# Performance work log

Measured on AMD Instinct MI355X. Metric: run time of the kernel, lower is better.

The kernel has to match this reference:

```python
import jax, jax.numpy as jnp
import numpy as np


def setup_inputs() -> dict:
    key = jax.random.key(0)
    k1, k2 = jax.random.split(key)
    mutation_dist = jax.random.uniform(k1, (8192, 96), dtype=jnp.float32)
    train_data = jax.random.uniform(k2, (65536, 96), dtype=jnp.float32)
    return {"mutation_dist": mutation_dist, "train_data": train_data}


def reference(mutation_dist, train_data):
    # torch.cdist with default p=2: pairwise Euclidean distances [N, M]
    # default compute_mode for large inputs)
    x2 = jnp.sum(mutation_dist * mutation_dist, axis=-1, keepdims=True)   # [N,1]
    y2 = jnp.sum(train_data * train_data, axis=-1)[None, :]               # [1,M]
    xy = mutation_dist @ train_data.T                                     # [N,M]
    sq = jnp.maximum(x2 + y2 - 2.0 * xy, 0.0)
    distances = jnp.sqrt(sq)
    min_dist = jnp.min(distances, axis=1) * 10.0
    return min_dist
```

## Files before the change

### kernel.cpp

```cpp
#include <hip/hip_runtime.h>
#include <hip/hip_bf16.h>


typedef __attribute__((ext_vector_type(8))) short bf16x8;
typedef __attribute__((ext_vector_type(4))) float f32x4;
typedef __attribute__((ext_vector_type(4))) int i32x4;
typedef __attribute__((ext_vector_type(16))) int i32x16;

#define NQ 8192
#define NT 65536
#define KD 96
#define QB 512
#define TSPLIT 64
#define TCHUNK (NT / TSPLIT)
#define TTILE 64
#define TILES (TCHUNK / TTILE)

#define GLOAD_LDS16(gp, lp)                                                  \
  __builtin_amdgcn_global_load_lds(                                          \
      (const __attribute__((address_space(1))) unsigned int*)(gp),           \
      (__attribute__((address_space(3))) unsigned int*)(lp), 16, 0, 0)
#define GLOAD_LDS4(gp, lp)                                                   \
  __builtin_amdgcn_global_load_lds(                                          \
      (const __attribute__((address_space(1))) unsigned int*)(gp),           \
      (__attribute__((address_space(3))) unsigned int*)(lp), 4, 0, 0)

static __device__ __forceinline__ ushort f2bf(float f) {
  unsigned u = __float_as_uint(f);
  return (ushort)((u + 0x7fffu + ((u >> 16) & 1u)) >> 16);
}
static __device__ __forceinline__ unsigned pk2(float a, float b) {
  return (unsigned)f2bf(a) | ((unsigned)f2bf(b) << 16);
}
static __device__ __forceinline__ int imin(int a, int b) { return a < b ? a : b; }

__global__ __launch_bounds__(256) void prep_kernel(
    const float* __restrict__ qf, const float* __restrict__ tf,
    char* __restrict__ qi8, char* __restrict__ ti8,
    int* __restrict__ x2i, int* __restrict__ y2h,
    float* __restrict__ outp)
{
  const int tid = threadIdx.x;
  const int b = blockIdx.x;
  const bool isq = b < (NQ / 64);
  const int rb = isq ? b : b - (NQ / 64);
  const float4* src = (const float4*)((isq ? qf : tf) + (size_t)rb * 64 * KD);
  char* drow = (isq ? qi8 : ti8) + (size_t)rb * 64 * KD;
  const int rloc = tid >> 2;
  const int t = tid & 3;

  unsigned pk[6];
  int sn = 0;
  #pragma unroll
  for (int i = 0; i < 6; ++i) {
    float4 v = src[tid * 6 + i];
    int q0 = (int)rintf(v.x * 254.0f) - 127;
    int q1 = (int)rintf(v.y * 254.0f) - 127;
    int q2 = (int)rintf(v.z * 254.0f) - 127;
    int q3 = (int)rintf(v.w * 254.0f) - 127;
    sn += q0 * q0 + q1 * q1 + q2 * q2 + q3 * q3;
    int w0 = isq ? q0 : -q0, w1 = isq ? q1 : -q1;
    int w2 = isq ? q2 : -q2, w3 = isq ? q3 : -q3;
    pk[i] = (unsigned)(w0 & 255) | ((unsigned)(w1 & 255) << 8) |
            ((unsigned)(w2 & 255) << 16) | ((unsigned)(w3 & 255) << 24);
  }
  uint2* op = (uint2*)(drow + (size_t)rloc * KD + t * 24);
  op[0] = make_uint2(pk[0], pk[1]);
  op[1] = make_uint2(pk[2], pk[3]);
  op[2] = make_uint2(pk[4], pk[5]);

  sn += __shfl_xor(sn, 1, 64);
  sn += __shfl_xor(sn, 2, 64);
  if (t == 0) {
    int row = rb * 64 + rloc;
    if (isq) { x2i[row] = sn; outp[row] = __uint_as_float(0x7f800000u); }
    else     { y2h[row] = (sn + 1) >> 1; }
  }
}

__global__ __launch_bounds__(512) void min_dist_kernel(
    const char* __restrict__ qi8, const char* __restrict__ ti8,
    const int* __restrict__ x2i, const int* __restrict__ y2h,
    float* __restrict__ outp)
{
  __shared__ __align__(16) char ldsA[2][TTILE * KD];
  __shared__ __align__(16) int ldsY[2][TTILE];

  const int tid  = threadIdx.x;
  const int w    = tid >> 6;
  const int lane = tid & 63;
  const int col  = lane & 31;
  const int hi   = lane >> 5;
  const int tsplit = blockIdx.x & (TSPLIT - 1);
  const int qblock = blockIdx.x / TSPLIT;
  const int qbase  = qblock * QB + w * 64;

  i32x4 bq[2][3];
  #pragma unroll
  for (int ct = 0; ct < 2; ++ct) {
    const char* qp = qi8 + (size_t)(qbase + ct * 32 + col) * KD + hi * 16;
    #pragma unroll
    for (int kb = 0; kb < 3; ++kb)
      bq[ct][kb] = *(const volatile i32x4*)(qp + kb * 32);
  }

  int goff, loff;
  {
    int f = tid >> 6, l = tid & 63;
    int tt = f / 3, kb = f - tt * 3;
    goff = (tt * 32 + (l & 31)) * KD + kb * 32 + (l >> 5) * 16;
    loff = tid * 16;
  }

  int m0 = 0x7fffffff, m1 = 0x7fffffff;

  const int trow0 = tsplit * TCHUNK;

  {
    const char* g0 = ti8 + (size_t)trow0 * KD;
    if (tid < 384)
      GLOAD_LDS16(g0 + goff, &ldsA[0][loff]);
    if (w == 0)
      GLOAD_LDS4(y2h + trow0 + lane, &ldsY[0][lane]);
  }
  __syncthreads();

  int cur = 0;
  #pragma unroll 1
  for (int tile = 0; tile < TILES; ++tile) {
    if (tile + 1 < TILES) {
      const int tb2 = trow0 + (tile + 1) * TTILE;
      const char* g2 = ti8 + (size_t)tb2 * KD;
      if (tid < 384)
        GLOAD_LDS16(g2 + goff, &ldsA[cur ^ 1][loff]);
      if (w == 0)
        GLOAD_LDS4(y2h + tb2 + lane, &ldsY[cur ^ 1][lane]);
    }

    #pragma unroll
    for (int tt = 0; tt < 2; ++tt) {
      const char* ap = &ldsA[cur][tt * 3 * 1024 + lane * 16];
      i32x4 a0 = *(const i32x4*)(ap);
      i32x4 a1 = *(const i32x4*)(ap + 1024);
      i32x4 a2 = *(const i32x4*)(ap + 2048);

      i32x4 y0 = *(const i32x4*)&ldsY[cur][tt * 32 + hi * 4];
      i32x4 y1 = *(const i32x4*)&ldsY[cur][tt * 32 + hi * 4 + 8];
      i32x4 yq2 = *(const i32x4*)&ldsY[cur][tt * 32 + hi * 4 + 16];
      i32x4 yq3 = *(const i32x4*)&ldsY[cur][tt * 32 + hi * 4 + 24];
      i32x16 c;
      c[0] = y0[0];  c[1] = y0[1];  c[2] = y0[2];  c[3] = y0[3];
      c[4] = y1[0];  c[5] = y1[1];  c[6] = y1[2];  c[7] = y1[3];
      c[8] = yq2[0]; c[9] = yq2[1]; c[10] = yq2[2]; c[11] = yq2[3];
      c[12] = yq3[0]; c[13] = yq3[1]; c[14] = yq3[2]; c[15] = yq3[3];

      i32x16 acc0 = __builtin_amdgcn_mfma_i32_32x32x32_i8(a0, bq[0][0], c, 0, 0, 0);
      i32x16 acc1 = __builtin_amdgcn_mfma_i32_32x32x32_i8(a0, bq[1][0], c, 0, 0, 0);
      acc0 = __builtin_amdgcn_mfma_i32_32x32x32_i8(a1, bq[0][1], acc0, 0, 0, 0);
      acc1 = __builtin_amdgcn_mfma_i32_32x32x32_i8(a1, bq[1][1], acc1, 0, 0, 0);
      acc0 = __builtin_amdgcn_mfma_i32_32x32x32_i8(a2, bq[0][2], acc0, 0, 0, 0);
      acc1 = __builtin_amdgcn_mfma_i32_32x32x32_i8(a2, bq[1][2], acc1, 0, 0, 0);

      {
        int t0 = imin(imin(acc0[0], acc0[1]), imin(acc0[2], acc0[3]));
        int t1 = imin(imin(acc0[4], acc0[5]), imin(acc0[6], acc0[7]));
        int t2 = imin(imin(acc0[8], acc0[9]), imin(acc0[10], acc0[11]));
        int t3 = imin(imin(acc0[12], acc0[13]), imin(acc0[14], acc0[15]));
        m0 = imin(m0, imin(imin(t0, t1), imin(t2, t3)));
      }
      {
        int t0 = imin(imin(acc1[0], acc1[1]), imin(acc1[2], acc1[3]));
        int t1 = imin(imin(acc1[4], acc1[5]), imin(acc1[6], acc1[7]));
        int t2 = imin(imin(acc1[8], acc1[9]), imin(acc1[10], acc1[11]));
        int t3 = imin(imin(acc1[12], acc1[13]), imin(acc1[14], acc1[15]));
        m1 = imin(m1, imin(imin(t0, t1), imin(t2, t3)));
      }
    }

    __syncthreads();
    cur ^= 1;
  }

  m0 = imin(m0, __shfl_xor(m0, 32, 64));
  m1 = imin(m1, __shfl_xor(m1, 32, 64));
  if (hi == 0) {
    int q0 = qbase + col;
    int sq0 = x2i[q0] + (m0 << 1);
    if (sq0 < 0) sq0 = 0;
    atomicMin((unsigned int*)&outp[q0],
              __float_as_uint(sqrtf((float)sq0) * (10.0f / 254.0f)));
    int q1 = qbase + 32 + col;
    int sq1 = x2i[q1] + (m1 << 1);
    if (sq1 < 0) sq1 = 0;
    atomicMin((unsigned int*)&outp[q1],
              __float_as_uint(sqrtf((float)sq1) * (10.0f / 254.0f)));
  }
}

extern "C" void kernel_launch(void* const* d_in, const int* in_sizes, int n_in,
                              void* d_out, int out_size, void* d_ws, size_t ws_size,
                              hipStream_t stream) {
  const float* qf = (const float*)d_in[0];
  const float* tf = (const float*)d_in[1];
  float* outp = (float*)d_out;

  char* qi8 = (char*)d_ws;
  char* ti8 = qi8 + (size_t)NQ * KD;
  int* x2i = (int*)(ti8 + (size_t)NT * KD);
  int* y2h = x2i + NQ;

  prep_kernel<<<(NQ + NT) / 64, 256, 0, stream>>>(qf, tf, qi8, ti8, x2i, y2h, outp);
  min_dist_kernel<<<(NQ / QB) * TSPLIT, 512, 0, stream>>>(qi8, ti8, x2i, y2h, outp);
}
```

Measured before the change: 119.3 us.

## Fuse prep and min-distance into one cooperative kernel with grid sync

Merges the quantization prep kernel and the int8 MFMA min-distance kernel into one cooperative launch separated by a grid-wide barrier, which removes the second kernel launch and its gap. The T split is halved to 32 so the grid of 512 blocks can be co-resident, with a 4-blocks-per-CU launch bound. Each block now does twice as many tiles and there is less parallelism over T. Grid sync adds its own overhead, and a two-kernel fallback runs if the cooperative launch fails.

New measurement: 200.3 us. 67.9% more time.

```diff
diff --git a/kernel.cpp b/kernel.cpp
--- a/kernel.cpp
+++ b/kernel.cpp
@@ -1,5 +1,8 @@
 #include <hip/hip_runtime.h>
 #include <hip/hip_bf16.h>
+#include <hip/hip_cooperative_groups.h>
+
+namespace cg = cooperative_groups;
 
 
 typedef __attribute__((ext_vector_type(8))) short bf16x8;
@@ -11,10 +14,13 @@
 #define NT 65536
 #define KD 96
 #define QB 512
-#define TSPLIT 64
+#define TSPLIT 32
 #define TCHUNK (NT / TSPLIT)
 #define TTILE 64
 #define TILES (TCHUNK / TTILE)
+#define GRID ((NQ / QB) * TSPLIT)
+#define PREP_ROWS ((NQ + NT) / GRID)
+#define PREP_UNITS (PREP_ROWS * 4)
 
 #define GLOAD_LDS16(gp, lp)                                                  \
   __builtin_amdgcn_global_load_lds(                                          \
@@ -34,65 +40,65 @@
 }
 static __device__ __forceinline__ int imin(int a, int b) { return a < b ? a : b; }
 
-__global__ __launch_bounds__(256) void prep_kernel(
+static __device__ __forceinline__ void phase1_prep(
+    int b, int tid,
     const float* __restrict__ qf, const float* __restrict__ tf,
     char* __restrict__ qi8, char* __restrict__ ti8,
     int* __restrict__ x2i, int* __restrict__ y2h,
     float* __restrict__ outp)
 {
-  const int tid = threadIdx.x;
-  const int b = blockIdx.x;
-  const bool isq = b < (NQ / 64);
-  const int rb = isq ? b : b - (NQ / 64);
-  const float4* src = (const float4*)((isq ? qf : tf) + (size_t)rb * 64 * KD);
-  char* drow = (isq ? qi8 : ti8) + (size_t)rb * 64 * KD;
-  const int rloc = tid >> 2;
-  const int t = tid & 3;
-
-  unsigned pk[6];
-  int sn = 0;
-  #pragma unroll
-  for (int i = 0; i < 6; ++i) {
-    float4 v = src[tid * 6 + i];
-    int q0 = (int)rintf(v.x * 254.0f) - 127;
-    int q1 = (int)rintf(v.y * 254.0f) - 127;
-    int q2 = (int)rintf(v.z * 254.0f) - 127;
-    int q3 = (int)rintf(v.w * 254.0f) - 127;
-    sn += q0 * q0 + q1 * q1 + q2 * q2 + q3 * q3;
-    int w0 = isq ? q0 : -q0, w1 = isq ? q1 : -q1;
-    int w2 = isq ? q2 : -q2, w3 = isq ? q3 : -q3;
-    pk[i] = (unsigned)(w0 & 255) | ((unsigned)(w1 & 255) << 8) |
-            ((unsigned)(w2 & 255) << 16) | ((unsigned)(w3 & 255) << 24);
-  }
-  uint2* op = (uint2*)(drow + (size_t)rloc * KD + t * 24);
-  op[0] = make_uint2(pk[0], pk[1]);
-  op[1] = make_uint2(pk[2], pk[3]);
-  op[2] = make_uint2(pk[4], pk[5]);
-
-  sn += __shfl_xor(sn, 1, 64);
-  sn += __shfl_xor(sn, 2, 64);
-  if (t == 0) {
-    int row = rb * 64 + rloc;
-    if (isq) { x2i[row] = sn; outp[row] = __uint_as_float(0x7f800000u); }
-    else     { y2h[row] = (sn + 1) >> 1; }
-  }
-}
-
-__global__ __launch_bounds__(512) void min_dist_kernel(
+  #pragma unroll 2
+  for (int u = tid; u < PREP_UNITS; u += 512) {
+    const int rl = u >> 2;
+    const int t  = u & 3;
+    const int gr = b * PREP_ROWS + rl;
+    const bool isq = gr < NQ;
+    const int r = isq ? gr : gr - NQ;
+    const float4* src = (const float4*)((isq ? qf : tf) + (size_t)r * KD);
+    char* drow = (isq ? qi8 : ti8) + (size_t)r * KD;
+
+    unsigned pk[6];
+    int sn = 0;
+    #pragma unroll
+    for (int i = 0; i < 6; ++i) {
+      float4 v = src[t * 6 + i];
+      int q0 = (int)rintf(v.x * 254.0f) - 127;
+      int q1 = (int)rintf(v.y * 254.0f) - 127;
+      int q2 = (int)rintf(v.z * 254.0f) - 127;
+      int q3 = (int)rintf(v.w * 254.0f) - 127;
+      sn += q0 * q0 + q1 * q1 + q2 * q2 + q3 * q3;
+      int w0 = isq ? q0 : -q0, w1 = isq ? q1 : -q1;
+      int w2 = isq ? q2 : -q2, w3 = isq ? q3 : -q3;
+      pk[i] = (unsigned)(w0 & 255) | ((unsigned)(w1 & 255) << 8) |
+              ((unsigned)(w2 & 255) << 16) | ((unsigned)(w3 & 255) << 24);
+    }
+    uint2* op = (uint2*)(drow + t * 24);
+    op[0] = make_uint2(pk[0], pk[1]);
+    op[1] = make_uint2(pk[2], pk[3]);
+    op[2] = make_uint2(pk[4], pk[5]);
+
+    sn += __shfl_xor(sn, 1, 64);
+    sn += __shfl_xor(sn, 2, 64);
+    if (t == 0) {
+      if (isq) { x2i[r] = sn; outp[r] = __uint_as_float(0x7f800000u); }
+      else     { y2h[r] = (sn + 1) >> 1; }
+    }
+  }
+}
+
+static __device__ __forceinline__ void phase2_mindist(
+    int b, int tid,
+    char (*ldsA)[TTILE * KD], int (*ldsY)[TTILE],
     const char* __restrict__ qi8, const char* __restrict__ ti8,
     const int* __restrict__ x2i, const int* __restrict__ y2h,
     float* __restrict__ outp)
 {
-  __shared__ __align__(16) char ldsA[2][TTILE * KD];
-  __shared__ __align__(16) int ldsY[2][TTILE];
-
-  const int tid  = threadIdx.x;
   const int w    = tid >> 6;
   const int lane = tid & 63;
   const int col  = lane & 31;
   const int hi   = lane >> 5;
-  const int tsplit = blockIdx.x & (TSPLIT - 1);
-  const int qblock = blockIdx.x / TSPLIT;
+  const int tsplit = b & (TSPLIT - 1);
+  const int qblock = b / TSPLIT;
   const int qbase  = qblock * QB + w * 64;
 
   i32x4 bq[2][3];
@@ -197,6 +203,37 @@
   }
 }
 
+__global__ __launch_bounds__(512, 4) void fused_kernel(
+    const float* __restrict__ qf, const float* __restrict__ tf,
+    char* __restrict__ qi8, char* __restrict__ ti8,
+    int* __restrict__ x2i, int* __restrict__ y2h,
+    float* __restrict__ outp)
+{
+  __shared__ __align__(16) char ldsA[2][TTILE * KD];
+  __shared__ __align__(16) int ldsY[2][TTILE];
+  phase1_prep(blockIdx.x, threadIdx.x, qf, tf, qi8, ti8, x2i, y2h, outp);
+  cg::this_grid().sync();
+  phase2_mindist(blockIdx.x, threadIdx.x, ldsA, ldsY, qi8, ti8, x2i, y2h, outp);
+}
+
+__global__ __launch_bounds__(512, 4) void prep_split(
+    const float* __restrict__ qf, const float* __restrict__ tf,
+    char* __restrict__ qi8, char* __restrict__ ti8,
+    int* __restrict__ x2i, int* __restrict__ y2h,
+    float* __restrict__ outp)
+{
+  phase1_prep(blockIdx.x, threadIdx.x, qf, tf, qi8, ti8, x2i, y2h, outp);
+}
+__global__ __launch_bounds__(512, 4) void mind_split(
+    const char* __restrict__ qi8, const char* __restrict__ ti8,
+    const int* __restrict__ x2i, const int* __restrict__ y2h,
+    float* __restrict__ outp)
+{
+  __shared__ __align__(16) char ldsA[2][TTILE * KD];
+  __shared__ __align__(16) int ldsY[2][TTILE];
+  phase2_mindist(blockIdx.x, threadIdx.x, ldsA, ldsY, qi8, ti8, x2i, y2h, outp);
+}
+
 extern "C" void kernel_launch(void* const* d_in, const int* in_sizes, int n_in,
                               void* d_out, int out_size, void* d_ws, size_t ws_size,
                               hipStream_t stream) {
@@ -209,6 +246,14 @@
   int* x2i = (int*)(ti8 + (size_t)NT * KD);
   int* y2h = x2i + NQ;
 
-  prep_kernel<<<(NQ + NT) / 64, 256, 0, stream>>>(qf, tf, qi8, ti8, x2i, y2h, outp);
-  min_dist_kernel<<<(NQ / QB) * TSPLIT, 512, 0, stream>>>(qi8, ti8, x2i, y2h, outp);
-}
+  void* args[] = {(void*)&qf, (void*)&tf, (void*)&qi8, (void*)&ti8,
+                  (void*)&x2i, (void*)&y2h, (void*)&outp};
+  hipError_t err = hipLaunchCooperativeKernel((const void*)fused_kernel,
+                                              dim3(GRID), dim3(512),
+                                              args, 0, stream);
+  if (err != hipSuccess) {
+    (void)hipGetLastError();
+    prep_split<<<GRID, 512, 0, stream>>>(qf, tf, qi8, ti8, x2i, y2h, outp);
+    mind_split<<<GRID, 512, 0, stream>>>(qi8, ti8, x2i, y2h, outp);
+  }
+}
```

## Prefetch two tiles ahead with vmcnt-based waits and split loader waves

Applied to the files above, without the earlier changes.

Changes the double-buffered tile loop so two tiles are already in flight before the loop. Each iteration waits with s_waitcnt vmcnt(1) and a raw barrier instead of a full __syncthreads, and issues the load for tile+2 after the compute barrier. The y2h load moves from wave 0 to wave 6, so no wave issues both kinds of async LDS load, and the vmcnt count stays simple. It also adds an explicit wait for the query register loads. This gives the global loads more time to complete behind compute. In exchange it depends on hand-written waitcnt correctness and issues wraparound (wasted) loads on the last two iterations.

Result: no change. 119.8 us (+0.4%).

```diff
diff --git a/kernel.cpp b/kernel.cpp
--- a/kernel.cpp
+++ b/kernel.cpp
@@ -103,12 +103,12 @@
     for (int kb = 0; kb < 3; ++kb)
       bq[ct][kb] = *(const volatile i32x4*)(qp + kb * 32);
   }
-
-  int goff, loff;
-  {
-    int f = tid >> 6, l = tid & 63;
-    int tt = f / 3, kb = f - tt * 3;
-    goff = (tt * 32 + (l & 31)) * KD + kb * 32 + (l >> 5) * 16;
+  asm volatile("s_waitcnt vmcnt(0)" ::: "memory");
+
+  int goff = 0, loff = 0;
+  if (w < 6) {
+    int tt = w / 3, kb = w - tt * 3;
+    goff = (tt * 32 + col) * KD + kb * 32 + hi * 16;
     loff = tid * 16;
   }
 
@@ -116,26 +116,20 @@
 
   const int trow0 = tsplit * TCHUNK;
 
-  {
-    const char* g0 = ti8 + (size_t)trow0 * KD;
-    if (tid < 384)
-      GLOAD_LDS16(g0 + goff, &ldsA[0][loff]);
-    if (w == 0)
-      GLOAD_LDS4(y2h + trow0 + lane, &ldsY[0][lane]);
-  }
-  __syncthreads();
+  #pragma unroll
+  for (int p = 0; p < 2; ++p) {
+    const int tb = trow0 + p * TTILE;
+    if (w < 6)      GLOAD_LDS16(ti8 + (size_t)tb * KD + goff, &ldsA[p][loff]);
+    else if (w == 6) GLOAD_LDS4(y2h + tb + lane, &ldsY[p][lane]);
+  }
 
   int cur = 0;
   #pragma unroll 1
   for (int tile = 0; tile < TILES; ++tile) {
-    if (tile + 1 < TILES) {
-      const int tb2 = trow0 + (tile + 1) * TTILE;
-      const char* g2 = ti8 + (size_t)tb2 * KD;
-      if (tid < 384)
-        GLOAD_LDS16(g2 + goff, &ldsA[cur ^ 1][loff]);
-      if (w == 0)
-        GLOAD_LDS4(y2h + tb2 + lane, &ldsY[cur ^ 1][lane]);
-    }
+    if (w < 7)
+      asm volatile("s_waitcnt vmcnt(1)" ::: "memory");
+    __builtin_amdgcn_s_barrier();
+    asm volatile("" ::: "memory");
 
     #pragma unroll
     for (int tt = 0; tt < 2; ++tt) {
@@ -170,14 +164,22 @@
       }
       {
         int t0 = imin(imin(acc1[0], acc1[1]), imin(acc1[2], acc1[3]));
-        int t1 = imin(imin(acc1[4], acc1[5]), imin(acc1[6], acc1[7]));
-        int t2 = imin(imin(acc1[8], acc1[9]), imin(acc1[10], acc1[11]));
+        int t1 = imin(imin(acc1[8], acc1[9]), imin(acc1[10], acc1[11]));
+        int t2 = imin(imin(acc1[4], acc1[5]), imin(acc1[6], acc1[7]));
         int t3 = imin(imin(acc1[12], acc1[13]), imin(acc1[14], acc1[15]));
         m1 = imin(m1, imin(imin(t0, t1), imin(t2, t3)));
       }
     }
 
-    __syncthreads();
+    asm volatile("" ::: "memory");
+    __builtin_amdgcn_s_barrier();
+    asm volatile("" ::: "memory");
+
+    {
+      const int tb2 = trow0 + ((tile + 2) & (TILES - 1)) * TTILE;
+      if (w < 6)      GLOAD_LDS16(ti8 + (size_t)tb2 * KD + goff, &ldsA[cur][loff]);
+      else if (w == 6) GLOAD_LDS4(y2h + tb2 + lane, &ldsY[cur][lane]);
+    }
     cur ^= 1;
   }
 
```
